# Kernel optimization log

Hardware: AMD Instinct MI355X
Metric: run time of the kernel (lower is better)

## Reference

```python
import jax, jax.numpy as jnp
import numpy as np
from jax import lax

# hyperparams (match init_kwargs)
DIM = 192      # dim
QK = 192       # qk_dim
HEADS = 8
GS = 128       # group_size
MLP = 384      # mlp_dim
M = 64         # num_tokens
B, H, W = 4, 128, 128


def setup_inputs() -> dict:
    key = jax.random.key(0)
    ks = jax.random.split(key, 12)
    def n(k, sh, sc=0.02):
        return jax.random.normal(k, sh, dtype=jnp.float32) * sc
    return {
        "x": n(ks[0], (B, DIM, H, W), 1.0),
        "ln_g": jnp.ones((DIM,), jnp.float32),
        "ln_b": jnp.zeros((DIM,), jnp.float32),
        "Wq": n(ks[1], (DIM, QK)),
        "Wk": n(ks[2], (DIM, QK)),
        "Wv": n(ks[3], (DIM, DIM)),
        "Wproj": n(ks[4], (DIM, DIM)),
        "Wkg": n(ks[5], (DIM, QK)),      # IRCA global-key projection of means
        "Wvg": n(ks[6], (DIM, DIM)),     # IRCA global-value projection of means
        "means": n(ks[7], (M, DIM), 1.0),  # token dictionary buffer
        "Wconv": n(ks[8], (DIM, DIM)),   # 1x1 conv (no bias) as matrix
        "mlp_ln_g": jnp.ones((DIM,), jnp.float32),
        "mlp_ln_b": jnp.zeros((DIM,), jnp.float32),
        "W_fc1": n(ks[9], (DIM, MLP)),
        "dw": n(ks[10], (MLP, 1, 3, 3)),  # depthwise 3x3 in ConvFFN
        "W_fc2": n(ks[11], (MLP, DIM)),
    }


def _ln(x, g, b, eps=1e-5):
    mu = x.mean(-1, keepdims=True)
    var = ((x - mu) ** 2).mean(-1, keepdims=True)
    return (x - mu) * lax.rsqrt(var + eps) * g + b


def _attn(q, k, v):
    scale = q.shape[-1] ** -0.5
    s = jnp.einsum('...qd,...kd->...qk', q, k) * scale
    p = jax.nn.softmax(s, axis=-1)
    return jnp.einsum('...qk,...kd->...qd', p, v)


def reference(x, ln_g, ln_b, Wq, Wk, Wv, Wproj, Wkg, Wvg, means,
              Wconv, mlp_ln_g, mlp_ln_b, W_fc1, dw, W_fc2):
    b, C, h, w = x.shape
    N = h * w
    xt = x.reshape(b, C, N).transpose(0, 2, 1)          # b n c
    residual = xt
    xn = _ln(xt, ln_g, ln_b)

    # IRCA: per-head global K/V from the token dictionary (means)
    kg = (means @ Wkg).reshape(M, HEADS, QK // HEADS).transpose(1, 0, 2)   # h m dq
    vg = (means @ Wvg).reshape(M, HEADS, C // HEADS).transpose(1, 0, 2)    # h m dv

    # cluster assignment (no-grad): cosine sim to means, argsort by cluster id
    xs = lax.stop_gradient(xn)
    ms = lax.stop_gradient(means)
    xs_n = xs / (jnp.linalg.norm(xs, axis=-1, keepdims=True) + 1e-12)
    ms_n = ms / (jnp.linalg.norm(ms, axis=-1, keepdims=True) + 1e-12)
    belong = jnp.argmax(xs_n @ ms_n.T, axis=-1)          # b n
    idx = jnp.argsort(belong, axis=-1)                   # b n, cluster-sorted order

    # IASA: project, gather into cluster-sorted order
    q = jnp.take_along_axis(xn @ Wq, idx[:, :, None], axis=1)
    k = jnp.take_along_axis(xn @ Wk, idx[:, :, None], axis=1)
    v = jnp.take_along_axis(xn @ Wv, idx[:, :, None], axis=1)

    gs = min(N, GS)
    ng = (N + gs - 1) // gs
    pad_n = ng * gs - N
    pq = jnp.concatenate([q, q[:, N - pad_n:N][:, ::-1]], axis=1)
    pq = pq.reshape(b, ng, gs, HEADS, -1).transpose(0, 1, 3, 2, 4)  # b ng h gs dq

    def windows(t):
        tr = jnp.concatenate([t, t[:, N - pad_n - gs:N][:, ::-1]], axis=1)  # len ng*gs+gs
        t1 = tr[:, :ng * gs].reshape(b, ng, gs, -1)
        t2 = tr[:, gs:].reshape(b, ng, gs, -1)
        tw = jnp.concatenate([t1, t2], axis=2)           # b ng 2gs c
        return tw.reshape(b, ng, 2 * gs, HEADS, -1).transpose(0, 1, 3, 2, 4)

    kw, vw = windows(k), windows(v)
    out1 = _attn(pq, kw, vw)                             # local overlapping windows
    out2 = _attn(pq, kg[None, None], vg[None, None])     # global dictionary attention
    out = (out1 + out2).transpose(0, 1, 3, 2, 4).reshape(b, ng * gs, C)[:, :N]

    # scatter back to original token order (idx is a permutation)
    inv = jnp.argsort(idx, axis=-1)
    out = jnp.take_along_axis(out, inv[:, :, None], axis=1)
    out = (out @ Wproj) @ Wconv                           # proj + 1x1 conv (no bias)
    xt = residual + out

    # PreNorm ConvFFN: LN -> fc1 -> depthwise 3x3 -> GELU -> fc2, residual
    h1 = _ln(xt, mlp_ln_g, mlp_ln_b) @ W_fc1              # b n mlp
    himg = h1.transpose(0, 2, 1).reshape(b, MLP, h, w)
    dwc = lax.conv_general_dilated(himg, dw, (1, 1), 'SAME',
                                   feature_group_count=MLP,
                                   dimension_numbers=('NCHW', 'OIHW', 'NCHW'))
    h2 = jax.nn.gelu(dwc.reshape(b, MLP, N).transpose(0, 2, 1))
    xt = xt + h2 @ W_fc2
    return xt.transpose(0, 2, 1).reshape(b, C, h, w)
```

## Files before the change

kernel.cpp:

```cpp
#include <hip/hip_runtime.h>

using u16 = unsigned short;
using u32 = unsigned int;
typedef __attribute__((ext_vector_type(8))) short short8;
typedef __attribute__((ext_vector_type(4))) short s16x4;
typedef __attribute__((ext_vector_type(4))) float f32x4;
typedef __attribute__((ext_vector_type(2))) float f32x2;
typedef __attribute__((ext_vector_type(4))) u16 u16x4;
typedef __attribute__((ext_vector_type(4))) u32 u32x4;

constexpr int CB   = 4;
constexpr int CC   = 192;
constexpr int CN   = 16384;
constexpr int BN   = CB * CN;
constexpr int CMLP = 384;

__device__ __forceinline__ float b2f(u16 u){ return __uint_as_float(((u32)u) << 16); }
__device__ __forceinline__ u16 f2b(float f){
  u32 u = __float_as_uint(f);
  u32 r = (u + 0x7FFFu + ((u >> 16) & 1u)) >> 16;
  return (u16)r;
}
__device__ __forceinline__ short8 ld8(const u16* p) {
  s16x4 a = *(const s16x4*)p;
  s16x4 b = *(const s16x4*)(p + 4);
  short8 r;
  r[0]=a[0]; r[1]=a[1]; r[2]=a[2]; r[3]=a[3];
  r[4]=b[0]; r[5]=b[1]; r[6]=b[2]; r[7]=b[3];
  return r;
}
__device__ __forceinline__ u32 pk_bf16(float lo, float hi) {
  u32 r;
  asm("v_cvt_pk_bf16_f32 %0, %1, %2" : "=v"(r) : "v"(lo), "v"(hi));
  return r;
}
__device__ __forceinline__ float exp2_fast(float x) {
  float r;
  asm("v_exp_f32 %0, %1" : "=v"(r) : "v"(x));
  return r;
}

template<int SRCMAJ>
__global__ __launch_bounds__(256) void ln_k(const float* __restrict__ src,
    const float* __restrict__ gg, const float* __restrict__ bb, u16* __restrict__ out)
{
  __shared__ float t[64 * 193];
  __shared__ float sg[192], sb[192];
  __shared__ float smu[64], srs[64];
  const int tid = threadIdx.x;
  const int blk = blockIdx.x;
  const int b = blk >> 8;
  const int n0 = (blk & 255) * 64;
  if (tid < 192) { sg[tid] = gg[tid]; sb[tid] = bb[tid]; }
  if (SRCMAJ == 0) {
    const size_t sbase = ((size_t)b * CC) * CN + n0;
    #pragma unroll
    for (int it = 0; it < 48; ++it) {
      int c = it * 4 + (tid >> 6);
      int tok = tid & 63;
      t[tok * 193 + c] = src[sbase + (size_t)c * CN + tok];
    }
  } else {
    const size_t sbase = ((size_t)(b * CN + n0)) * CC;
    #pragma unroll
    for (int it = 0; it < 48; ++it) {
      int e = it * 256 + tid;
      int tok = e / 192, c = e % 192;
      t[tok * 193 + c] = src[sbase + (size_t)tok * CC + c];
    }
  }
  __syncthreads();
  {
    int tok = tid >> 2, sub = tid & 3;
    float s = 0.f, sq = 0.f;
    #pragma unroll
    for (int i = 0; i < 48; ++i) {
      float v = t[tok * 193 + sub * 48 + i];
      s += v; sq += v * v;
    }
    s  += __shfl_xor(s, 1);  s  += __shfl_xor(s, 2);
    sq += __shfl_xor(sq, 1); sq += __shfl_xor(sq, 2);
    float mu = s * (1.f / 192.f);
    float var = fmaxf(sq * (1.f / 192.f) - mu * mu, 0.f);
    float rs = rsqrtf(var + 1e-5f);
    if (sub == 0) { smu[tok] = mu; srs[tok] = rs; }
  }
  __syncthreads();
  const size_t obase = ((size_t)(b * CN + n0)) * CC;
  #pragma unroll
  for (int it = 0; it < 48; ++it) {
    int e = it * 256 + tid;
    int tk = e / 192, c = e % 192;
    float v = (t[tk * 193 + c] - smu[tk]) * srs[tk] * sg[c] + sb[c];
    out[obase + (size_t)tk * CC + c] = f2b(v);
  }
}

__global__ __launch_bounds__(192) void prep_means_k(const float* __restrict__ means,
    const float* __restrict__ Wkg, const float* __restrict__ Wvg,
    u16* __restrict__ msnT, float* __restrict__ kg, float* __restrict__ vg)
{
  __shared__ float sv[192];
  __shared__ float red[192];
  const int m = blockIdx.x, c = threadIdx.x;
  float v = means[m * 192 + c];
  sv[c] = v; red[c] = v * v;
  __syncthreads();
  for (int s = 96; s >= 3; s >>= 1) {
    if (c < s) red[c] += red[c + s];
    __syncthreads();
  }
  if (c == 0) red[0] = 1.f / (sqrtf(red[0] + red[1] + red[2]) + 1e-12f);
  __syncthreads();
  float scale = red[0];
  msnT[m * 192 + c] = f2b(v * scale);
  float a1 = 0.f, a2 = 0.f;
  for (int cc = 0; cc < 192; ++cc) {
    float mv = sv[cc];
    a1 += mv * Wkg[cc * 192 + c];
    a2 += mv * Wvg[cc * 192 + c];
  }
  int h = c / 24, d = c % 24;
  kg[h * (64 * 24) + m * 24 + d] = a1;
  vg[h * (64 * 24) + m * 24 + d] = a2;
}

__global__ __launch_bounds__(256) void wpcT_k(const float* __restrict__ Wp,
    const float* __restrict__ Wc, u16* __restrict__ WpcT)
{
  int e = blockIdx.x * 256 + threadIdx.x;
  if (e >= 192 * 192) return;
  int i = e / 192, j = e % 192;
  float a = 0.f;
  for (int k = 0; k < 192; ++k) a += Wp[i * 192 + k] * Wc[k * 192 + j];
  WpcT[j * 192 + i] = f2b(a);
}

__global__ __launch_bounds__(256) void wT_k(const float* __restrict__ W,
    u16* __restrict__ dst, int K, int NCsrc, int jcount)
{
  int e = blockIdx.x * 256 + threadIdx.x;
  if (e >= K * jcount) return;
  int j = e / K, k = e % K;
  dst[e] = f2b(W[k * NCsrc + j]);
}

enum { EP_QKV = 0, EP_ARGMAX = 1, EP_RESID = 2, EP_H1 = 3, EP_FINAL = 4 };

template<int KTOT, int NCOLS, int EPI>
__global__ __launch_bounds__(256) void gemm3_k(const u16* __restrict__ A,
    const u16* __restrict__ Wt, const float* __restrict__ resid,
    void* __restrict__ outp, int astride)
{
  __shared__ __attribute__((aligned(16))) u16 lA[64 * 200];
  constexpr int KC = KTOT / 192;
  constexpr int WCOLS = NCOLS / 4;
  constexpr int WCT = WCOLS / 16;
  constexpr int NACC = (KC == 2) ? WCT * 4 : 4;
  const int tid = threadIdx.x;
  const int row0 = blockIdx.x * 64;
  const int b = row0 >> 14;
  const int wv = tid >> 6, lane = tid & 63;
  const int l15 = lane & 15, g4 = lane >> 4, q8 = g4 * 8;
  const int colw = wv * WCOLS;

  f32x4 acc[NACC];
  #pragma unroll
  for (int i = 0; i < NACC; ++i) acc[i] = 0.f;

  #pragma unroll
  for (int kc = 0; kc < KC; ++kc) {
    if (kc) __syncthreads();
    #pragma unroll
    for (int it = 0; it < 12; ++it) {
      int e4 = (it * 256 + tid) * 4;
      int r = e4 / 192, k = e4 % 192;
      u16x4 v = *(const u16x4*)(A + (size_t)(row0 + r) * astride + kc * 192 + k);
      *(u16x4*)(lA + r * 200 + k) = v;
    }
    __syncthreads();
    short8 af[4][6];
    #pragma unroll
    for (int rt = 0; rt < 4; ++rt)
      #pragma unroll
      for (int ks = 0; ks < 6; ++ks)
        af[rt][ks] = *(const short8*)(lA + (rt * 16 + l15) * 200 + ks * 32 + q8);

    #pragma unroll
    for (int jc = 0; jc < WCT; ++jc) {
      const u16* pW = Wt + (size_t)(colw + jc * 16 + l15) * KTOT + kc * 192 + q8;
      short8 wf[6];
      #pragma unroll
      for (int ks = 0; ks < 6; ++ks) wf[ks] = *(const short8*)(pW + ks * 32);
      #pragma unroll
      for (int ks = 0; ks < 6; ++ks)
        #pragma unroll
        for (int rt = 0; rt < 4; ++rt) {
          int ai = (KC == 2) ? jc * 4 + rt : rt;
          acc[ai] = __builtin_amdgcn_mfma_f32_16x16x32_bf16(af[rt][ks], wf[ks], acc[ai], 0, 0, 0);
        }

      if (KC == 1 && EPI == EP_QKV) {
        u16* o = (u16*)outp;
        int col = colw + jc * 16 + l15;
        #pragma unroll
        for (int rt = 0; rt < 4; ++rt) {
          int row = row0 + rt * 16 + g4 * 4;
          #pragma unroll
          for (int r = 0; r < 4; ++r)
            o[(size_t)(row + r) * 576 + col] = f2b(acc[rt][r]);
          acc[rt] = 0.f;
        }
      } else if (KC == 1 && EPI == EP_H1) {
        u16* o = (u16*)outp;
        int col = colw + jc * 16 + l15;
        #pragma unroll
        for (int rt = 0; rt < 4; ++rt) {
          int row = row0 + rt * 16 + g4 * 4;
          #pragma unroll
          for (int r = 0; r < 4; ++r)
            o[(size_t)(row + r) * CMLP + col] = f2b(acc[rt][r]);
          acc[rt] = 0.f;
        }
      } else if (KC == 1 && EPI == EP_RESID) {
        float* o = (float*)outp;
        int col = colw + jc * 16 + l15;
        size_t cb = ((size_t)(b * CC + col)) * CN;
        #pragma unroll
        for (int rt = 0; rt < 4; ++rt) {
          int row = row0 + rt * 16 + g4 * 4;
          #pragma unroll
          for (int r = 0; r < 4; ++r) {
            int n = (row + r) & 16383;
            o[(size_t)(row + r) * CC + col] = resid[cb + n] + acc[rt][r];
          }
          acc[rt] = 0.f;
        }
      }
    }
  }

  if (EPI == EP_ARGMAX) {
    __syncthreads();
    float* sMax = (float*)lA;
    int*   sIdx = (int*)(lA + 512);
    #pragma unroll
    for (int rt = 0; rt < 4; ++rt)
      #pragma unroll
      for (int r = 0; r < 4; ++r) {
        float bv = acc[rt][r]; int bi = wv * 16 + l15;
        #pragma unroll
        for (int d = 1; d < 16; d <<= 1) {
          float ov = __shfl_xor(bv, d);
          int   oi = __shfl_xor(bi, d);
          if (ov > bv || (ov == bv && oi < bi)) { bv = ov; bi = oi; }
        }
        if (l15 == 0) {
          int row = rt * 16 + g4 * 4 + r;
          sMax[wv * 64 + row] = bv;
          sIdx[wv * 64 + row] = bi;
        }
      }
    __syncthreads();
    if (tid < 64) {
      float bv = -3e38f; int bi = 0;
      #pragma unroll
      for (int w = 0; w < 4; ++w) {
        float v = sMax[w * 64 + tid]; int ci = sIdx[w * 64 + tid];
        if (v > bv || (v == bv && ci < bi)) { bv = v; bi = ci; }
      }
      ((int*)outp)[row0 + tid] = bi;
    }
  } else if (EPI == EP_FINAL) {
    float* o = (float*)outp;
    #pragma unroll
    for (int jc = 0; jc < WCT; ++jc) {
      int col = colw + jc * 16 + l15;
      size_t cb = ((size_t)(b * CC + col)) * CN;
      #pragma unroll
      for (int rt = 0; rt < 4; ++rt) {
        int row = row0 + rt * 16 + g4 * 4;
        #pragma unroll
        for (int r = 0; r < 4; ++r) {
          int n = (row + r) & 16383;
          o[cb + n] = resid[(size_t)(row + r) * CC + col] + acc[jc * 4 + rt][r];
        }
      }
    }
  }
}

__global__ __launch_bounds__(256) void hist_k(const int* __restrict__ belong, int* __restrict__ histG)
{
  __shared__ int h[64];
  int tid = threadIdx.x, blk = blockIdx.x;
  if (tid < 64) h[tid] = 0;
  __syncthreads();
  int c = belong[blk * 256 + tid];
  atomicAdd(&h[c], 1);
  __syncthreads();
  if (tid < 64) histG[blk * 64 + tid] = h[tid];
}

__global__ __launch_bounds__(64) void scan_k(const int* __restrict__ histG, int* __restrict__ chunkBase)
{
  int b = blockIdx.x, c = threadIdx.x;
  int tot = 0;
  for (int ch = 0; ch < 64; ++ch) tot += histG[(b * 64 + ch) * 64 + c];
  int inc = tot;
  for (int d = 1; d < 64; d <<= 1) {
    int v = __shfl_up(inc, d);
    if (c >= d) inc += v;
  }
  int run = inc - tot;
  for (int ch = 0; ch < 64; ++ch) {
    chunkBase[(b * 64 + ch) * 64 + c] = run;
    run += histG[(b * 64 + ch) * 64 + c];
  }
}

__global__ __launch_bounds__(256) void rank_k(const int* __restrict__ belong,
    const int* __restrict__ chunkBase, int* __restrict__ idx)
{
  __shared__ int WH[4][64];
  int tid = threadIdx.x, blk = blockIdx.x;
  int b = blk >> 6, chl = blk & 63;
  int wv = tid >> 6, lane = tid & 63;
  ((int*)WH)[tid] = 0;
  __syncthreads();
  int nl = chl * 256 + tid;
  int c = belong[blk * 256 + tid];
  int rank = 0;
  for (int m = 0; m < 64; ++m) {
    unsigned long long msk = __ballot(c == m);
    if (c == m) {
      rank = __popcll(msk & ((1ull << lane) - 1ull));
      if (rank == 0) WH[wv][m] = __popcll(msk);
    }
  }
  __syncthreads();
  int off = 0;
  #pragma unroll
  for (int w = 0; w < 3; ++w) if (w < wv) off += WH[w][c];
  int pos = chunkBase[(b * 64 + chl) * 64 + c] + off + rank;
  idx[b * CN + pos] = nl;
}

__global__ __launch_bounds__(256) void attn_k(u16* __restrict__ qkv,
    const float* __restrict__ kg, const float* __restrict__ vg,
    const int* __restrict__ idx)
{
  __shared__ __attribute__((aligned(16))) u16 sK[320 * 28];
  __shared__ __attribute__((aligned(16))) u16 sVT[24 * 340];
  __shared__ int sidx[256];
  const int g = blockIdx.x, h = blockIdx.y, b = blockIdx.z;
  const int tid = threadIdx.x;
  const int wave = tid >> 6, lane = tid & 63;
  const int l15 = lane & 15, g4 = lane >> 4;
  const int q8 = g4 * 8;
  const size_t base = (size_t)b * CN * 576;
  const float QSC = 0.20412414523193154f * 1.4426950408889634f;
  short8 z8 = {0,0,0,0,0,0,0,0};

  {
    int p = g * 128 + tid;
    if (p >= CN) p = 2 * CN - 1 - p;
    sidx[tid] = idx[b * CN + p];
  }
  __syncthreads();

  #pragma unroll
  for (int it = 0; it < 8; ++it) {
    int e4 = (it * 256 + tid) * 4;
    if (e4 < 7680) {
      int r = e4 / 24, c = e4 % 24;
      if (r < 256) {
        int p = sidx[r];
        *(u16x4*)(sK + r * 28 + c) =
          *(const u16x4*)(qkv + base + (size_t)p * 576 + 192 + h * 24 + c);
      } else {
        const float* kp = kg + h * 1536 + (r - 256) * 24 + c;
        u16x4 o;
        o[0] = f2b(kp[0]); o[1] = f2b(kp[1]); o[2] = f2b(kp[2]); o[3] = f2b(kp[3]);
        *(u16x4*)(sK + r * 28 + c) = o;
      }
    }
  }
  #pragma unroll
  for (int it = 0; it < 8; ++it) {
    int e4 = (it * 256 + tid) * 4;
    if (e4 < 7680) {
      int kk = e4 / 24, c = e4 % 24;
      if (kk < 256) {
        int p = sidx[kk];
        u16x4 v = *(const u16x4*)(qkv + base + (size_t)p * 576 + 384 + h * 24 + c);
        sVT[(c + 0) * 340 + kk] = v[0];
        sVT[(c + 1) * 340 + kk] = v[1];
        sVT[(c + 2) * 340 + kk] = v[2];
        sVT[(c + 3) * 340 + kk] = v[3];
      } else {
        const float* vp = vg + h * 1536 + (kk - 256) * 24 + c;
        sVT[(c + 0) * 340 + kk] = f2b(vp[0]);
        sVT[(c + 1) * 340 + kk] = f2b(vp[1]);
        sVT[(c + 2) * 340 + kk] = f2b(vp[2]);
        sVT[(c + 3) * 340 + kk] = f2b(vp[3]);
      }
    }
  }

  short8 qf[2];
  #pragma unroll
  for (int rt = 0; rt < 2; ++rt) {
    int qrow = sidx[wave * 32 + rt * 16 + l15];
    if (g4 < 3) {
      short8 raw = ld8(qkv + base + (size_t)qrow * 576 + h * 24 + q8);
      u32x4 qq;
      #pragma unroll
      for (int j = 0; j < 4; ++j) {
        float lo = b2f((u16)raw[2 * j]) * QSC;
        float hi = b2f((u16)raw[2 * j + 1]) * QSC;
        qq[j] = pk_bf16(lo, hi);
      }
      qf[rt] = __builtin_bit_cast(short8, qq);
    } else {
      qf[rt] = z8;
    }
  }
  __syncthreads();

  float l1[2] = {0.f, 0.f}, l2[2] = {0.f, 0.f};
  f32x4 O1[2][2], O2[2][2];
  #pragma unroll
  for (int rt = 0; rt < 2; ++rt)
    #pragma unroll
    for (int ct2 = 0; ct2 < 2; ++ct2) { O1[rt][ct2] = 0.f; O2[rt][ct2] = 0.f; }

  const int srow = (lane & 48) + ((lane & 48) >> 2);
  const int srcLo = ((lane & 16) << 1) + l15;
  const int srcHi = srcLo + 16;
  const bool hiSel = lane >= 32;
  f32x4 zz = 0.f;

  auto do_tile = [&](int ktile, float* l, f32x4 (*O)[2]) {
    short8 aK[4];
    #pragma unroll
    for (int ct = 0; ct < 4; ++ct)
      aK[ct] = (g4 < 3) ? ld8(sK + (ktile + ct * 16 + l15) * 28 + q8) : z8;
    short8 bV[2][2];
    #pragma unroll
    for (int kc = 0; kc < 2; ++kc)
      #pragma unroll
      for (int ct2 = 0; ct2 < 2; ++ct2) {
        int vrow = ct2 * 16 + l15;
        bV[kc][ct2] = (vrow < 24) ? ld8(sVT + vrow * 340 + ktile + kc * 32 + q8) : z8;
      }
    #pragma unroll
    for (int rt = 0; rt < 2; ++rt) {
      f32x4 p[4];
      #pragma unroll
      for (int ct = 0; ct < 4; ++ct)
        p[ct] = __builtin_amdgcn_mfma_f32_16x16x32_bf16(aK[ct], qf[rt], zz, 0, 0, 0);
      float ps = 0.f;
      #pragma unroll
      for (int ct = 0; ct < 4; ++ct)
        #pragma unroll
        for (int r = 0; r < 4; ++r) {
          float pe = exp2_fast(p[ct][r]);
          p[ct][r] = pe;
          ps += pe;
        }
      ps += __shfl_xor(ps, 16);
      ps += __shfl_xor(ps, 32);
      l[rt] += ps;
      #pragma unroll
      for (int kc = 0; kc < 2; ++kc) {
        u32 wA0 = pk_bf16(p[kc * 2][0], p[kc * 2][1]);
        u32 wA1 = pk_bf16(p[kc * 2][2], p[kc * 2][3]);
        u32 wB0 = pk_bf16(p[kc * 2 + 1][0], p[kc * 2 + 1][1]);
        u32 wB1 = pk_bf16(p[kc * 2 + 1][2], p[kc * 2 + 1][3]);
        u32 a0 = (u32)__shfl((int)wA0, srcLo), a1 = (u32)__shfl((int)wA1, srcLo);
        u32 a2 = (u32)__shfl((int)wA0, srcHi), a3 = (u32)__shfl((int)wA1, srcHi);
        u32 b0 = (u32)__shfl((int)wB0, srcLo), b1 = (u32)__shfl((int)wB1, srcLo);
        u32 b2 = (u32)__shfl((int)wB0, srcHi), b3 = (u32)__shfl((int)wB1, srcHi);
        u32x4 fr;
        fr[0] = hiSel ? b0 : a0; fr[1] = hiSel ? b1 : a1;
        fr[2] = hiSel ? b2 : a2; fr[3] = hiSel ? b3 : a3;
        short8 aP = __builtin_bit_cast(short8, fr);
        #pragma unroll
        for (int ct2 = 0; ct2 < 2; ++ct2)
          O[rt][ct2] = __builtin_amdgcn_mfma_f32_16x16x32_bf16(aP, bV[kc][ct2], O[rt][ct2], 0, 0, 0);
      }
    }
  };

  do_tile(0,   l1, O1);
  do_tile(64,  l1, O1);
  do_tile(128, l1, O1);
  do_tile(192, l1, O1);
  do_tile(256, l2, O2);

  #pragma unroll
  for (int rt = 0; rt < 2; ++rt) {
    float li1 = 1.f / l1[rt];
    float li2 = 1.f / l2[rt];
    #pragma unroll
    for (int r = 0; r < 4; ++r) {
      float i1 = __shfl(li1, srow + r);
      float i2 = __shfl(li2, srow + r);
      int tok = sidx[wave * 32 + rt * 16 + g4 * 4 + r];
      #pragma unroll
      for (int ct2 = 0; ct2 < 2; ++ct2) {
        int d = ct2 * 16 + l15;
        if (d < 24) {
          float v = O1[rt][ct2][r] * i1 + O2[rt][ct2][r] * i2;
          qkv[base + (size_t)tok * 576 + h * 24 + d] = f2b(v);
        }
      }
    }
  }
}

__global__ __launch_bounds__(256) void conv_k(const u16* __restrict__ h1,
    const float* __restrict__ dw, u16* __restrict__ h2g)
{
  __shared__ float t[1156 * 10];
  __shared__ float sdw[72];
  const int tile = blockIdx.x;
  const int jg = blockIdx.y;
  const int bb = blockIdx.z;
  const int y0 = (tile >> 2) * 32, x0 = (tile & 3) * 32;
  const int tid = threadIdx.x;
  if (tid < 72) sdw[tid] = dw[jg * 72 + tid];
  #pragma unroll
  for (int it = 0; it < 5; ++it) {
    int e = it * 256 + tid;
    if (e < 1156) {
      int yy = e / 34 - 1 + y0, xx = e % 34 - 1 + x0;
      float v[8];
      if (yy >= 0 && yy < 128 && xx >= 0 && xx < 128) {
        short8 raw = *(const short8*)(h1 + ((size_t)(bb * CN + yy * 128 + xx)) * CMLP + jg * 8);
        #pragma unroll
        for (int c = 0; c < 8; ++c) v[c] = b2f((u16)raw[c]);
      } else {
        #pragma unroll
        for (int c = 0; c < 8; ++c) v[c] = 0.f;
      }
      #pragma unroll
      for (int c = 0; c < 8; c += 2) {
        f32x2 p; p[0] = v[c]; p[1] = v[c + 1];
        *(f32x2*)(t + e * 10 + c) = p;
      }
    }
  }
  __syncthreads();
  float acc[4][8];
  #pragma unroll
  for (int px = 0; px < 4; ++px)
    #pragma unroll
    for (int c = 0; c < 8; ++c) acc[px][c] = 0.f;
  #pragma unroll
  for (int k = 0; k < 9; ++k) {
    const int dy = k / 3, dx = k % 3;
    float w[8];
    #pragma unroll
    for (int c = 0; c < 8; ++c) w[c] = sdw[c * 9 + k];
    #pragma unroll
    for (int px = 0; px < 4; ++px) {
      int idx2 = px * 256 + tid;
      int oy = idx2 >> 5, ox = idx2 & 31;
      const float* vp = t + ((oy + dy) * 34 + ox + dx) * 10;
      #pragma unroll
      for (int c = 0; c < 8; ++c) acc[px][c] += vp[c] * w[c];
    }
  }
  #pragma unroll
  for (int px = 0; px < 4; ++px) {
    int idx2 = px * 256 + tid;
    int oy = idx2 >> 5, ox = idx2 & 31;
    short8 o;
    #pragma unroll
    for (int c = 0; c < 8; ++c) {
      float a = acc[px][c];
      float u = 1.5957691216057308f * (a + 0.044715f * a * a * a);
      float gel = a / (1.f + __expf(-u));
      o[c] = (short)f2b(gel);
    }
    *(short8*)(h2g + ((size_t)(bb * CN + (y0 + oy) * 128 + x0 + ox)) * CMLP + jg * 8) = o;
  }
}

extern "C" void kernel_launch(void* const* d_in, const int* in_sizes, int n_in,
                              void* d_out, int out_size, void* d_ws, size_t ws_size,
                              hipStream_t stream)
{
  const float* x     = (const float*)d_in[0];
  const float* ln_g  = (const float*)d_in[1];
  const float* ln_b  = (const float*)d_in[2];
  const float* Wq    = (const float*)d_in[3];
  const float* Wk    = (const float*)d_in[4];
  const float* Wv    = (const float*)d_in[5];
  const float* Wproj = (const float*)d_in[6];
  const float* Wkg   = (const float*)d_in[7];
  const float* Wvg   = (const float*)d_in[8];
  const float* means = (const float*)d_in[9];
  const float* Wconv = (const float*)d_in[10];
  const float* mlp_g = (const float*)d_in[11];
  const float* mlp_b = (const float*)d_in[12];
  const float* Wfc1  = (const float*)d_in[13];
  const float* dw    = (const float*)d_in[14];
  const float* Wfc2  = (const float*)d_in[15];
  float* out = (float*)d_out;
  (void)in_sizes; (void)n_in; (void)out_size; (void)ws_size;

  char* ws = (char*)d_ws;
  size_t off = 0;
  auto alloc = [&](size_t sz) { void* p = ws + off; off += (sz + 255) & ~(size_t)255; return p; };
  u16*  xn    = (u16*)alloc((size_t)BN * 192 * 2);
  u16*  qkv   = (u16*)alloc((size_t)BN * 576 * 2);
  float* xt2  = (float*)alloc((size_t)BN * 192 * 4);
  u16*  h2g   = (u16*)alloc((size_t)BN * 384 * 2);
  u16*  msnT  = (u16*)alloc(64 * 192 * 2);
  u16*  WqkvT = (u16*)alloc(576 * 192 * 2);
  u16*  WpcT  = (u16*)alloc(192 * 192 * 2);
  u16*  Wfc1T = (u16*)alloc(384 * 192 * 2);
  u16*  Wfc2T = (u16*)alloc(192 * 384 * 2);
  float* kg   = (float*)alloc(8 * 64 * 24 * 4);
  float* vg   = (float*)alloc(8 * 64 * 24 * 4);
  int*  belong = (int*)alloc(BN * 4);
  int*  idxb   = (int*)alloc(BN * 4);
  int*  histG  = (int*)alloc(256 * 64 * 4);
  int*  chunkBase = (int*)alloc(256 * 64 * 4);
  u16* ln2 = xn;
  u16* h1  = qkv;

  prep_means_k<<<64, 192, 0, stream>>>(means, Wkg, Wvg, msnT, kg, vg);
  wpcT_k<<<144, 256, 0, stream>>>(Wproj, Wconv, WpcT);
  wT_k<<<144, 256, 0, stream>>>(Wq, WqkvT + 0,             192, 192, 192);
  wT_k<<<144, 256, 0, stream>>>(Wk, WqkvT + 192 * 192,     192, 192, 192);
  wT_k<<<144, 256, 0, stream>>>(Wv, WqkvT + 2 * 192 * 192, 192, 192, 192);
  wT_k<<<288, 256, 0, stream>>>(Wfc1, Wfc1T, 192, 384, 384);
  wT_k<<<288, 256, 0, stream>>>(Wfc2, Wfc2T, 384, 192, 192);

  ln_k<0><<<1024, 256, 0, stream>>>(x, ln_g, ln_b, xn);
  gemm3_k<192, 64, EP_ARGMAX><<<1024, 256, 0, stream>>>(xn, msnT, nullptr, belong, 192);
  hist_k<<<256, 256, 0, stream>>>(belong, histG);
  scan_k<<<4, 64, 0, stream>>>(histG, chunkBase);
  rank_k<<<256, 256, 0, stream>>>(belong, chunkBase, idxb);
  gemm3_k<192, 576, EP_QKV><<<1024, 256, 0, stream>>>(xn, WqkvT, nullptr, qkv, 192);
  attn_k<<<dim3(128, 8, 4), 256, 0, stream>>>(qkv, kg, vg, idxb);
  gemm3_k<192, 192, EP_RESID><<<1024, 256, 0, stream>>>(qkv, WpcT, x, xt2, 576);
  ln_k<1><<<1024, 256, 0, stream>>>(xt2, mlp_g, mlp_b, ln2);
  gemm3_k<192, 384, EP_H1><<<1024, 256, 0, stream>>>(ln2, Wfc1T, nullptr, h1, 192);
  conv_k<<<dim3(16, 48, 4), 256, 0, stream>>>(h1, dw, h2g);
  gemm3_k<384, 192, EP_FINAL><<<1024, 256, 0, stream>>>(h2g, Wfc2T, xt2, out, 384);
}
```

Measured before the change: 370.4 us.

## Fuse cluster argmax into layernorm, split GEMM columns across grid, transpose final epilogue

```diff
diff --git a/kernel.cpp b/kernel.cpp
--- a/kernel.cpp
+++ b/kernel.cpp
@@ -42,7 +42,8 @@
 
 template<int SRCMAJ>
 __global__ __launch_bounds__(256) void ln_k(const float* __restrict__ src,
-    const float* __restrict__ gg, const float* __restrict__ bb, u16* __restrict__ out)
+    const float* __restrict__ gg, const float* __restrict__ bb, u16* __restrict__ out,
+    const u16* __restrict__ msnT, int* __restrict__ belong)
 {
   __shared__ float t[64 * 193];
   __shared__ float sg[192], sb[192];
@@ -94,6 +95,55 @@
     float v = (t[tk * 193 + c] - smu[tk]) * srs[tk] * sg[c] + sb[c];
     out[obase + (size_t)tk * CC + c] = f2b(v);
   }
+
+  if (SRCMAJ == 0) {
+    const int wv = tid >> 6, lane = tid & 63;
+    const int l15 = lane & 15, g4 = lane >> 4, q8 = g4 * 8;
+    const int tok = wv * 16 + l15;
+    const float mu = smu[tok], rs = srs[tok];
+    short8 afm[6];
+    #pragma unroll
+    for (int ks = 0; ks < 6; ++ks) {
+      u32x4 qq;
+      #pragma unroll
+      for (int j = 0; j < 4; ++j) {
+        int c = ks * 32 + q8 + 2 * j;
+        float v0 = (t[tok * 193 + c]     - mu) * rs * sg[c]     + sb[c];
+        float v1 = (t[tok * 193 + c + 1] - mu) * rs * sg[c + 1] + sb[c + 1];
+        qq[j] = pk_bf16(v0, v1);
+      }
+      afm[ks] = __builtin_bit_cast(short8, qq);
+    }
+    f32x4 sacc[4];
+    #pragma unroll
+    for (int ct = 0; ct < 4; ++ct) {
+      sacc[ct] = 0.f;
+      const u16* pM = msnT + (ct * 16 + l15) * 192 + q8;
+      short8 mf[6];
+      #pragma unroll
+      for (int ks = 0; ks < 6; ++ks) mf[ks] = *(const short8*)(pM + ks * 32);
+      #pragma unroll
+      for (int ks = 0; ks < 6; ++ks)
+        sacc[ct] = __builtin_amdgcn_mfma_f32_16x16x32_bf16(afm[ks], mf[ks], sacc[ct], 0, 0, 0);
+    }
+    #pragma unroll
+    for (int r = 0; r < 4; ++r) {
+      float bv = -3e38f; int bi = 1 << 30;
+      #pragma unroll
+      for (int ct = 0; ct < 4; ++ct) {
+        float v = sacc[ct][r];
+        int ci = ct * 16 + l15;
+        if (v > bv || (v == bv && ci < bi)) { bv = v; bi = ci; }
+      }
+      #pragma unroll
+      for (int d = 1; d < 16; d <<= 1) {
+        float ov = __shfl_xor(bv, d);
+        int   oi = __shfl_xor(bi, d);
+        if (ov > bv || (ov == bv && oi < bi)) { bv = ov; bi = oi; }
+      }
+      if (l15 == 0) belong[b * CN + n0 + wv * 16 + g4 * 4 + r] = bi;
+    }
+  }
 }
 
 __global__ __launch_bounds__(192) void prep_means_k(const float* __restrict__ means,
@@ -145,7 +195,7 @@
   dst[e] = f2b(W[k * NCsrc + j]);
 }
 
-enum { EP_QKV = 0, EP_ARGMAX = 1, EP_RESID = 2, EP_H1 = 3, EP_FINAL = 4 };
+enum { EP_QKV = 0, EP_RESID = 2, EP_H1 = 3, EP_FINAL = 4 };
 
 template<int KTOT, int NCOLS, int EPI>
 __global__ __launch_bounds__(256) void gemm3_k(const u16* __restrict__ A,
@@ -158,11 +208,12 @@
   constexpr int WCT = WCOLS / 16;
   constexpr int NACC = (KC == 2) ? WCT * 4 : 4;
   const int tid = threadIdx.x;
-  const int row0 = blockIdx.x * 64;
+  const int row0 = blockIdx.y * 64;
   const int b = row0 >> 14;
+  const int col0 = blockIdx.x * NCOLS;
   const int wv = tid >> 6, lane = tid & 63;
   const int l15 = lane & 15, g4 = lane >> 4, q8 = g4 * 8;
-  const int colw = wv * WCOLS;
+  const int colw = col0 + wv * WCOLS;
 
   f32x4 acc[NACC];
   #pragma unroll
@@ -197,7 +248,10 @@
         #pragma unroll
         for (int rt = 0; rt < 4; ++rt) {
           int ai = (KC == 2) ? jc * 4 + rt : rt;
-          acc[ai] = __builtin_amdgcn_mfma_f32_16x16x32_bf16(af[rt][ks], wf[ks], acc[ai], 0, 0, 0);
+          if (EPI == EP_FINAL)
+            acc[ai] = __builtin_amdgcn_mfma_f32_16x16x32_bf16(wf[ks], af[rt][ks], acc[ai], 0, 0, 0);
+          else
+            acc[ai] = __builtin_amdgcn_mfma_f32_16x16x32_bf16(af[rt][ks], wf[ks], acc[ai], 0, 0, 0);
         }
 
       if (KC == 1 && EPI == EP_QKV) {
@@ -240,53 +294,21 @@
     }
   }
 
-  if (EPI == EP_ARGMAX) {
-    __syncthreads();
-    float* sMax = (float*)lA;
-    int*   sIdx = (int*)(lA + 512);
-    #pragma unroll
-    for (int rt = 0; rt < 4; ++rt)
-      #pragma unroll
-      for (int r = 0; r < 4; ++r) {
-        float bv = acc[rt][r]; int bi = wv * 16 + l15;
-        #pragma unroll
-        for (int d = 1; d < 16; d <<= 1) {
-          float ov = __shfl_xor(bv, d);
-          int   oi = __shfl_xor(bi, d);
-          if (ov > bv || (ov == bv && oi < bi)) { bv = ov; bi = oi; }
+  if (EPI == EP_FINAL) {
+    float* o = (float*)outp;
+    #pragma unroll
+    for (int jc = 0; jc < WCT; ++jc)
+      #pragma unroll
+      for (int tt = 0; tt < 4; ++tt) {
+        int token = row0 + tt * 16 + l15;
+        int n = token & 16383;
+        #pragma unroll
+        for (int r = 0; r < 4; ++r) {
+          int outcol = colw + jc * 16 + g4 * 4 + r;
+          o[((size_t)(b * CC + outcol)) * CN + n] =
+              resid[(size_t)token * CC + outcol] + acc[jc * 4 + tt][r];
         }
-        if (l15 == 0) {
-          int row = rt * 16 + g4 * 4 + r;
-          sMax[wv * 64 + row] = bv;
-          sIdx[wv * 64 + row] = bi;
-        }
-      }
-    __syncthreads();
-    if (tid < 64) {
-      float bv = -3e38f; int bi = 0;
-      #pragma unroll
-      for (int w = 0; w < 4; ++w) {
-        float v = sMax[w * 64 + tid]; int ci = sIdx[w * 64 + tid];
-        if (v > bv || (v == bv && ci < bi)) { bv = v; bi = ci; }
-      }
-      ((int*)outp)[row0 + tid] = bi;
-    }
-  } else if (EPI == EP_FINAL) {
-    float* o = (float*)outp;
-    #pragma unroll
-    for (int jc = 0; jc < WCT; ++jc) {
-      int col = colw + jc * 16 + l15;
-      size_t cb = ((size_t)(b * CC + col)) * CN;
-      #pragma unroll
-      for (int rt = 0; rt < 4; ++rt) {
-        int row = row0 + rt * 16 + g4 * 4;
-        #pragma unroll
-        for (int r = 0; r < 4; ++r) {
-          int n = (row + r) & 16383;
-          o[cb + n] = resid[(size_t)(row + r) * CC + col] + acc[jc * 4 + rt][r];
-        }
-      }
-    }
+      }
   }
 }
 
@@ -641,16 +663,15 @@
   wT_k<<<288, 256, 0, stream>>>(Wfc1, Wfc1T, 192, 384, 384);
   wT_k<<<288, 256, 0, stream>>>(Wfc2, Wfc2T, 384, 192, 192);
 
-  ln_k<0><<<1024, 256, 0, stream>>>(x, ln_g, ln_b, xn);
-  gemm3_k<192, 64, EP_ARGMAX><<<1024, 256, 0, stream>>>(xn, msnT, nullptr, belong, 192);
+  ln_k<0><<<1024, 256, 0, stream>>>(x, ln_g, ln_b, xn, msnT, belong);
   hist_k<<<256, 256, 0, stream>>>(belong, histG);
   scan_k<<<4, 64, 0, stream>>>(histG, chunkBase);
   rank_k<<<256, 256, 0, stream>>>(belong, chunkBase, idxb);
-  gemm3_k<192, 576, EP_QKV><<<1024, 256, 0, stream>>>(xn, WqkvT, nullptr, qkv, 192);
+  gemm3_k<192, 192, EP_QKV><<<dim3(3, 1024), 256, 0, stream>>>(xn, WqkvT, nullptr, qkv, 192);
   attn_k<<<dim3(128, 8, 4), 256, 0, stream>>>(qkv, kg, vg, idxb);
-  gemm3_k<192, 192, EP_RESID><<<1024, 256, 0, stream>>>(qkv, WpcT, x, xt2, 576);
-  ln_k<1><<<1024, 256, 0, stream>>>(xt2, mlp_g, mlp_b, ln2);
-  gemm3_k<192, 384, EP_H1><<<1024, 256, 0, stream>>>(ln2, Wfc1T, nullptr, h1, 192);
+  gemm3_k<192, 192, EP_RESID><<<dim3(1, 1024), 256, 0, stream>>>(qkv, WpcT, x, xt2, 576);
+  ln_k<1><<<1024, 256, 0, stream>>>(xt2, mlp_g, mlp_b, ln2, nullptr, nullptr);
+  gemm3_k<192, 192, EP_H1><<<dim3(2, 1024), 256, 0, stream>>>(ln2, Wfc1T, nullptr, h1, 192);
   conv_k<<<dim3(16, 48, 4), 256, 0, stream>>>(h1, dw, h2g);
-  gemm3_k<384, 192, EP_FINAL><<<1024, 256, 0, stream>>>(h2g, Wfc2T, xt2, out, 384);
-}
+  gemm3_k<384, 192, EP_FINAL><<<dim3(1, 1024), 256, 0, stream>>>(h2g, Wfc2T, xt2, out, 384);
+}
```

Result: no change. 372.4 us (+0.5%).
